# Kernel optimization log

Measured on AMD Instinct MI355X. Metric: run time of the kernel, lower is better.

Reference implementation:

```python
import jax, jax.numpy as jnp
import numpy as np

L, B, T, D, H = 8, 4, 1024, 1024, 16
DH = D // H
TPB, NB = 16, 64  # tokens_per_block, max_blocks; T == TPB*NB
EPS = 1e-5


def _block_causal_mask():
    idx = jnp.arange(T)
    causal = idx[:, None] >= idx[None, :]
    blk = idx // TPB
    block_diag = blk[:, None] == blk[None, :]
    return causal | block_diag  # [T, T] bool


def _ln(x, g, b):
    mu = jnp.mean(x, axis=-1, keepdims=True)
    var = jnp.mean(jnp.square(x - mu), axis=-1, keepdims=True)
    return (x - mu) * jax.lax.rsqrt(var + EPS) * g + b


def setup_inputs() -> dict:
    key = jax.random.key(0)
    ks = jax.random.split(key, 8)
    s = 0.02
    inp = {
        'sequences': jax.random.normal(ks[0], (B, T, D), jnp.float32),
        'Wq': jax.random.normal(ks[1], (L, D, D), jnp.float32) * s,
        'bq': jnp.zeros((L, D), jnp.float32),
        'Wk': jax.random.normal(ks[2], (L, D, D), jnp.float32) * s,
        'bk': jnp.zeros((L, D), jnp.float32),
        'Wv': jax.random.normal(ks[3], (L, D, D), jnp.float32) * s,
        'bv': jnp.zeros((L, D), jnp.float32),
        'Wp': jax.random.normal(ks[4], (L, D, D), jnp.float32) * s,
        'bp': jnp.zeros((L, D), jnp.float32),
        'ln1_g': jnp.ones((L, D), jnp.float32),
        'ln1_b': jnp.zeros((L, D), jnp.float32),
        'ln2_g': jnp.ones((L, D), jnp.float32),
        'ln2_b': jnp.zeros((L, D), jnp.float32),
        'W1': jax.random.normal(ks[5], (L, D, 4 * D), jnp.float32) * s,
        'b1': jnp.zeros((L, 4 * D), jnp.float32),
        'W2': jax.random.normal(ks[6], (L, 4 * D, D), jnp.float32) * s,
        'b2': jnp.zeros((L, D), jnp.float32),
        'lnf_g': jnp.ones((D,), jnp.float32),
        'lnf_b': jnp.zeros((D,), jnp.float32),
    }
    return inp


def reference(sequences, Wq, bq, Wk, bk, Wv, bv, Wp, bp,
              ln1_g, ln1_b, ln2_g, ln2_b, W1, b1, W2, b2, lnf_g, lnf_b):
    mask = _block_causal_mask()
    scale = 1.0 / np.sqrt(DH)
    x = sequences
    for i in range(L):
        h = _ln(x, ln1_g[i], ln1_b[i])
        q = (h @ Wq[i] + bq[i]).reshape(B, T, H, DH)
        k = (h @ Wk[i] + bk[i]).reshape(B, T, H, DH)
        v = (h @ Wv[i] + bv[i]).reshape(B, T, H, DH)
        att = jnp.einsum('bthd,bshd->bhts', q, k) * scale  # [B,H,T,T]
        att = jnp.where(mask, att, -jnp.inf)
        att = jax.nn.softmax(att, axis=-1)
        y = jnp.einsum('bhts,bshd->bthd', att, v).reshape(B, T, D)
        x = x + (y @ Wp[i] + bp[i])
        h2 = _ln(x, ln2_g[i], ln2_b[i])
        ff = jax.nn.gelu(h2 @ W1[i] + b1[i], approximate=False) @ W2[i] + b2[i]
        x = x + ff
    return _ln(x, lnf_g, lnf_b)
```

## Files before the change

kernel.cpp:

```cpp
#include <hip/hip_runtime.h>
#include <hip/hip_bf16.h>
#include <math.h>

#define B_ 4
#define T_ 1024
#define D_ 1024
#define H_ 16
#define DH_ 64
#define M_ 4096
#define QSTR_ 3072
#define EPS_ 1e-5f

typedef __attribute__((ext_vector_type(4))) float f32x4;
typedef __attribute__((ext_vector_type(8))) short s16x8;

#if __has_builtin(__builtin_amdgcn_exp2f)
#define EXP2F __builtin_amdgcn_exp2f
#else
#define EXP2F exp2f
#endif

__device__ __forceinline__ float gelu_f(float x) {
  return 0.5f * x * (1.0f + erff(x * 0.70710678118654752f));
}
__device__ __forceinline__ float b2f(unsigned short u) {
  union { unsigned int i; float f; } c; c.i = ((unsigned int)u) << 16; return c.f;
}
__device__ __forceinline__ unsigned short f2b(float f) {
  __hip_bfloat16 h = __float2bfloat16(f);
  return *reinterpret_cast<unsigned short*>(&h);
}
__device__ __forceinline__ void g2l16(void* l, const void* g) {
  __builtin_amdgcn_global_load_lds(
      (const __attribute__((address_space(1))) void*)g,
      (__attribute__((address_space(3))) void*)l, 16, 0, 0);
}

template<bool BF16OUT>
__global__ __launch_bounds__(256) void ln_kernel(
    const float* __restrict__ in, void* __restrict__ out,
    const float* __restrict__ g, const float* __restrict__ b) {
  const int row = blockIdx.x;
  const int tid = threadIdx.x;
  const float* rp = in + (size_t)row * D_;
  float4 v = *reinterpret_cast<const float4*>(rp + tid * 4);
  float s = v.x + v.y + v.z + v.w;
  float s2 = v.x * v.x + v.y * v.y + v.z * v.z + v.w * v.w;
#pragma unroll
  for (int off = 1; off < 64; off <<= 1) {
    s += __shfl_xor(s, off);
    s2 += __shfl_xor(s2, off);
  }
  __shared__ float red[2][4];
  const int wid = tid >> 6;
  if ((tid & 63) == 0) { red[0][wid] = s; red[1][wid] = s2; }
  __syncthreads();
  s = red[0][0] + red[0][1] + red[0][2] + red[0][3];
  s2 = red[1][0] + red[1][1] + red[1][2] + red[1][3];
  const float mu = s * (1.0f / D_);
  const float var = s2 * (1.0f / D_) - mu * mu;
  const float rs = rsqrtf(var + EPS_);
  float4 gv = *reinterpret_cast<const float4*>(g + tid * 4);
  float4 bv = *reinterpret_cast<const float4*>(b + tid * 4);
  float o0 = (v.x - mu) * rs * gv.x + bv.x;
  float o1 = (v.y - mu) * rs * gv.y + bv.y;
  float o2 = (v.z - mu) * rs * gv.z + bv.z;
  float o3 = (v.w - mu) * rs * gv.w + bv.w;
  if (BF16OUT) {
    ushort4 pk;
    pk.x = f2b(o0); pk.y = f2b(o1); pk.z = f2b(o2); pk.w = f2b(o3);
    *reinterpret_cast<ushort4*>((unsigned short*)out + (size_t)row * D_ + tid * 4) = pk;
  } else {
    *reinterpret_cast<float4*>((float*)out + (size_t)row * D_ + tid * 4) =
        make_float4(o0, o1, o2, o3);
  }
}

__global__ __launch_bounds__(256) void concat_bias(
    const float* __restrict__ bq, const float* __restrict__ bk,
    const float* __restrict__ bv, float* __restrict__ out) {
  const int i = blockIdx.x * 256 + threadIdx.x;
  const int l = i / QSTR_, c = i % QSTR_;
  const float* src = (c < 1024) ? bq : ((c < 2048) ? bk : bv);
  out[i] = src[l * 1024 + (c & 1023)];
}

__global__ __launch_bounds__(256) void reduce_add(
    float* __restrict__ x, const float* __restrict__ p) {
  const int i = blockIdx.x * 256 + threadIdx.x;
  float4 a = reinterpret_cast<float4*>(x)[i];
  float4 b = reinterpret_cast<const float4*>(p)[i];
  a.x += b.x; a.y += b.y; a.z += b.z; a.w += b.w;
  reinterpret_cast<float4*>(x)[i] = a;
}

__device__ __forceinline__ void transpose_tile(
    const float* __restrict__ src, int sld,
    __hip_bfloat16* __restrict__ dst, int dld, int k0, int n0) {
  __shared__ float tile[32][33];
  const int t = threadIdx.x;
  const int r = t >> 3;
  const int cq = (t & 7) * 4;
  float4 vv = *reinterpret_cast<const float4*>(src + (size_t)(k0 + r) * sld + n0 + cq);
  tile[r][cq + 0] = vv.x; tile[r][cq + 1] = vv.y;
  tile[r][cq + 2] = vv.z; tile[r][cq + 3] = vv.w;
  __syncthreads();
  ushort4 o;
  o.x = f2b(tile[cq + 0][r]); o.y = f2b(tile[cq + 1][r]);
  o.z = f2b(tile[cq + 2][r]); o.w = f2b(tile[cq + 3][r]);
  *reinterpret_cast<ushort4*>((unsigned short*)dst + (size_t)(n0 + r) * dld + k0 + cq) = o;
}

struct TrAll {
  const float *wq, *wk, *wv, *wp, *w1, *w2;
  __hip_bfloat16 *dqkv, *dp, *d1, *d2;
};

__global__ __launch_bounds__(256) void transpose_all(TrAll a) {
  const int t = blockIdx.x;
  const float* src;
  __hip_bfloat16* dst;
  int sld, dld, k0, n0;
  if (t < 4096) {
    const int m = t >> 10, tile = t & 1023;
    k0 = (tile >> 5) * 32; n0 = (tile & 31) * 32;
    src = (m == 0) ? a.wq : (m == 1) ? a.wk : (m == 2) ? a.wv : a.wp;
    sld = 1024; dld = 1024;
    dst = (m < 3) ? (a.dqkv + (size_t)m * 1024 * 1024) : a.dp;
  } else if (t < 8192) {
    const int tile = t - 4096;
    k0 = (tile & 31) * 32; n0 = (tile >> 5) * 32;
    src = a.w1; sld = 4096; dst = a.d1; dld = 1024;
  } else {
    const int tile = t - 8192;
    k0 = (tile >> 5) * 32; n0 = (tile & 31) * 32;
    src = a.w2; sld = 1024; dst = a.d2; dld = 4096;
  }
  transpose_tile(src, sld, dst, dld, k0, n0);
}

template<int MODE, int BN>
__global__ __launch_bounds__(256) void gemm_mfma(
    const __hip_bfloat16* __restrict__ A,
    const __hip_bfloat16* __restrict__ Bt,
    const float* __restrict__ bias,
    void* __restrict__ Cout, int N, int K) {
  __shared__ short As[3][128 * 32];
  __shared__ short Bs[3][BN * 32];
  int bid = blockIdx.y * gridDim.x + blockIdx.x;
  const int nwg = gridDim.x * gridDim.y;
  bid = (bid & 7) * (nwg >> 3) + (bid >> 3);
  const int gn = (bid % gridDim.x) * BN;
  const int gm = (bid / gridDim.x) * 128;

  const int tid = threadIdx.x;
  const int wid = tid >> 6, lane = tid & 63;
  constexpr int MR = (BN == 128) ? 4 : 2;
  const int wm = (BN == 128) ? (wid >> 1) : wid;
  const int wn = (BN == 128) ? (wid & 1) : 0;
  const int fr = lane & 15, kg = lane >> 4;

  const int ldr = lane >> 2;
  const int ldk = (((lane & 3) ^ ((lane >> 3) & 3)) * 8);
  const unsigned short* ap =
      (const unsigned short*)A + (size_t)(gm + wid * 32 + ldr) * K + ldk;
  const unsigned short* bp =
      (const unsigned short*)Bt +
      (size_t)(gn + ((BN == 128) ? wid * 32 : wid * 16) + ldr) * K + ldk;

  const int nkt = K >> 5;

#define STAGE_T(t, buf)                                                    \
  {                                                                        \
    const unsigned short* a_ = ap + (size_t)(t) * 32;                      \
    g2l16((char*)As[buf] + (wid * 2) * 1024, a_);                          \
    g2l16((char*)As[buf] + (wid * 2 + 1) * 1024, a_ + (size_t)16 * K);     \
    const unsigned short* b_ = bp + (size_t)(t) * 32;                      \
    if (BN == 128) {                                                       \
      g2l16((char*)Bs[buf] + (wid * 2) * 1024, b_);                        \
      g2l16((char*)Bs[buf] + (wid * 2 + 1) * 1024, b_ + (size_t)16 * K);   \
    } else {                                                               \
      g2l16((char*)Bs[buf] + wid * 1024, b_);                              \
    }                                                                      \
  }

  STAGE_T(0, 0);
  STAGE_T(1, 1);

  const int cxa = (kg ^ ((fr >> 1) & 3)) * 8;
  f32x4 acc[MR][4] = {};
  for (int t = 0; t < nkt; ++t) {
    const int buf = t % 3;
    if (t + 2 < nkt) STAGE_T(t + 2, (t + 2) % 3);
    const int rem = nkt - 1 - t;
    if (rem >= 2) {
      if (BN == 128) asm volatile("s_waitcnt vmcnt(8)" ::: "memory");
      else           asm volatile("s_waitcnt vmcnt(6)" ::: "memory");
    } else if (rem == 1) {
      if (BN == 128) asm volatile("s_waitcnt vmcnt(4)" ::: "memory");
      else           asm volatile("s_waitcnt vmcnt(3)" ::: "memory");
    } else {
      asm volatile("s_waitcnt vmcnt(0)" ::: "memory");
    }
    __builtin_amdgcn_s_barrier();
    __builtin_amdgcn_sched_barrier(0);
    s16x8 af[MR], bfr[4];
#pragma unroll
    for (int m = 0; m < MR; ++m)
      af[m] = *reinterpret_cast<const s16x8*>(
          &As[buf][(wm * (16 * MR) + m * 16 + fr) * 32 + cxa]);
#pragma unroll
    for (int n = 0; n < 4; ++n)
      bfr[n] = *reinterpret_cast<const s16x8*>(
          &Bs[buf][(wn * 64 + n * 16 + fr) * 32 + cxa]);
#pragma unroll
    for (int m = 0; m < MR; ++m)
#pragma unroll
      for (int n = 0; n < 4; ++n)
        acc[m][n] = __builtin_amdgcn_mfma_f32_16x16x32_bf16(af[m], bfr[n], acc[m][n], 0, 0, 0);
    __builtin_amdgcn_sched_barrier(0);
    __builtin_amdgcn_s_barrier();
  }
#undef STAGE_T

  const int r0 = gm + wm * (16 * MR);
  const int c0 = gn + wn * 64;
  float bb[4];
#pragma unroll
  for (int n = 0; n < 4; ++n)
    bb[n] = bias ? bias[c0 + n * 16 + fr] : 0.0f;
#pragma unroll
  for (int m = 0; m < MR; ++m) {
#pragma unroll
    for (int j = 0; j < 4; ++j) {
      const int row = r0 + m * 16 + kg * 4 + j;
#pragma unroll
      for (int n = 0; n < 4; ++n) {
        float val = acc[m][n][j] + bb[n];
        const size_t idx = (size_t)row * N + c0 + n * 16 + fr;
        if (MODE == 0) {
          ((unsigned short*)Cout)[idx] = f2b(val);
        } else if (MODE == 1) {
          float* cp = (float*)Cout + idx;
          *cp = *cp + val;
        } else {
          ((unsigned short*)Cout)[idx] = f2b(gelu_f(val));
        }
      }
    }
  }
}

__global__ __launch_bounds__(256) void gemm_sk2(
    const __hip_bfloat16* __restrict__ A,
    const __hip_bfloat16* __restrict__ Bt,
    const float* __restrict__ bias,
    float* __restrict__ X, float* __restrict__ P,
    int N, int K , int KS ) {
  __shared__ short As[3][128 * 32];
  __shared__ short Bs[3][64 * 32];
  int bid = blockIdx.y * gridDim.x + blockIdx.x;
  const int nwg = gridDim.x * gridDim.y;
  bid = (bid & 7) * (nwg >> 3) + (bid >> 3);
  const int gn = (bid % gridDim.x) * 64;
  const int gm = (bid / gridDim.x) * 128;
  const int koff = blockIdx.z * KS;

  const int tid = threadIdx.x;
  const int wid = tid >> 6, lane = tid & 63;
  const int wm = wid, wn = 0;
  const int fr = lane & 15, kg = lane >> 4;

  const int ldr = lane >> 2;
  const int ldk = (((lane & 3) ^ ((lane >> 3) & 3)) * 8);
  const unsigned short* ap =
      (const unsigned short*)A + (size_t)(gm + wid * 32 + ldr) * K + koff + ldk;
  const unsigned short* bp =
      (const unsigned short*)Bt + (size_t)(gn + wid * 16 + ldr) * K + koff + ldk;

  const int nkt = KS >> 5;

#define STAGE_S(t, buf)                                                    \
  {                                                                        \
    const unsigned short* a_ = ap + (size_t)(t) * 32;                      \
    g2l16((char*)As[buf] + (wid * 2) * 1024, a_);                          \
    g2l16((char*)As[buf] + (wid * 2 + 1) * 1024, a_ + (size_t)16 * K);     \
    g2l16((char*)Bs[buf] + wid * 1024, bp + (size_t)(t) * 32);             \
  }

  STAGE_S(0, 0);
  STAGE_S(1, 1);

  const int cxa = (kg ^ ((fr >> 1) & 3)) * 8;
  f32x4 acc[2][4] = {};
  for (int t = 0; t < nkt; ++t) {
    const int buf = t % 3;
    if (t + 2 < nkt) STAGE_S(t + 2, (t + 2) % 3);
    const int rem = nkt - 1 - t;
    if (rem >= 2)      asm volatile("s_waitcnt vmcnt(6)" ::: "memory");
    else if (rem == 1) asm volatile("s_waitcnt vmcnt(3)" ::: "memory");
    else               asm volatile("s_waitcnt vmcnt(0)" ::: "memory");
    __builtin_amdgcn_s_barrier();
    __builtin_amdgcn_sched_barrier(0);
    s16x8 af[2], bfr[4];
#pragma unroll
    for (int m = 0; m < 2; ++m)
      af[m] = *reinterpret_cast<const s16x8*>(
          &As[buf][(wm * 32 + m * 16 + fr) * 32 + cxa]);
#pragma unroll
    for (int n = 0; n < 4; ++n)
      bfr[n] = *reinterpret_cast<const s16x8*>(
          &Bs[buf][(wn * 64 + n * 16 + fr) * 32 + cxa]);
#pragma unroll
    for (int m = 0; m < 2; ++m)
#pragma unroll
      for (int n = 0; n < 4; ++n)
        acc[m][n] = __builtin_amdgcn_mfma_f32_16x16x32_bf16(af[m], bfr[n], acc[m][n], 0, 0, 0);
    __builtin_amdgcn_sched_barrier(0);
    __builtin_amdgcn_s_barrier();
  }
#undef STAGE_S

  const int r0 = gm + wm * 32;
  const int c0 = gn;
  if (blockIdx.z == 0) {
    float bb[4];
#pragma unroll
    for (int n = 0; n < 4; ++n) bb[n] = bias[c0 + n * 16 + fr];
#pragma unroll
    for (int m = 0; m < 2; ++m)
#pragma unroll
      for (int j = 0; j < 4; ++j) {
        const int row = r0 + m * 16 + kg * 4 + j;
#pragma unroll
        for (int n = 0; n < 4; ++n) {
          const size_t idx = (size_t)row * N + c0 + n * 16 + fr;
          X[idx] = X[idx] + acc[m][n][j] + bb[n];
        }
      }
  } else {
#pragma unroll
    for (int m = 0; m < 2; ++m)
#pragma unroll
      for (int j = 0; j < 4; ++j) {
        const int row = r0 + m * 16 + kg * 4 + j;
#pragma unroll
        for (int n = 0; n < 4; ++n) {
          const size_t idx = (size_t)row * N + c0 + n * 16 + fr;
          P[idx] = acc[m][n][j];
        }
      }
  }
}

__global__ __launch_bounds__(256) void attn_mfma(
    const __hip_bfloat16* __restrict__ qkv, __hip_bfloat16* __restrict__ yg) {
  const int qb = 7 - blockIdx.x;
  const int hh = blockIdx.y;
  const int bb = blockIdx.z;
  __shared__ short Qs[128 * 64];
  __shared__ short Ks[64 * 64];
  __shared__ short Vt[64 * 64];
  const int tid = threadIdx.x;
  const int wid = tid >> 6, lane = tid & 63;
  const int fr = lane & 15, kg = lane >> 4;
  const size_t qb_base = (size_t)bb * T_ * QSTR_ + (size_t)hh * DH_;
  const unsigned short* qgp = (const unsigned short*)qkv + qb_base;
  const unsigned short* kgp = qgp + 1024;
  const unsigned short* vgp = qgp + 2048;
  const float C = 0.125f * 1.4426950408889634f;

  {
    const int r8 = lane >> 3, cp = lane & 7;
#pragma unroll
    for (int u = 0; u < 4; ++u) {
      const int row = wid * 32 + u * 8 + r8;
      const int c16 = cp ^ (row & 7);
      g2l16((char*)Qs + (wid * 32 + u * 8) * 128,
            qgp + (size_t)(qb * 128 + row) * QSTR_ + c16 * 8);
    }
  }
  asm volatile("s_waitcnt vmcnt(0)" ::: "memory");
  __syncthreads();
  s16x8 qf[2][2];
#pragma unroll
  for (int rg = 0; rg < 2; ++rg) {
    const int row = wid * 32 + rg * 16 + fr;
    const char* rp = (const char*)Qs + row * 128;
    qf[rg][0] = *reinterpret_cast<const s16x8*>(rp + (((0 + kg) ^ (row & 7)) << 4));
    qf[rg][1] = *reinterpret_cast<const s16x8*>(rp + (((4 + kg) ^ (row & 7)) << 4));
  }

  f32x4 acco[2][4] = {};
  float m_run[2][4], l_run[2][4];
#pragma unroll
  for (int rg = 0; rg < 2; ++rg)
#pragma unroll
    for (int j = 0; j < 4; ++j) { m_run[rg][j] = -INFINITY; l_run[rg][j] = 0.f; }

  const int q16hi = qb * 8 + wid * 2 + 1;
  const int ntile = 2 * qb + 2;
  for (int kt = 0; kt < ntile; ++kt) {
    __syncthreads();
    {
      const int r8 = lane >> 3, cp = lane & 7;
#pragma unroll
      for (int u = 0; u < 2; ++u) {
        const int row = wid * 16 + u * 8 + r8;
        const int c16 = cp ^ (row & 7);
        g2l16((char*)Ks + (wid * 16 + u * 8) * 128,
              kgp + (size_t)(kt * 64 + row) * QSTR_ + c16 * 8);
      }
    }
    {
      const int kv0 = tid >> 3;
      const int d0 = (tid & 7) * 8;
      const int rot = tid & 7;
#pragma unroll
      for (int u = 0; u < 2; ++u) {
        const int kv = u * 32 + kv0;
        s16x8 sv = *reinterpret_cast<const s16x8*>(
            vgp + (size_t)(kt * 64 + kv) * QSTR_ + d0);
#pragma unroll
        for (int j = 0; j < 8; ++j) {
          const int jj = (j + rot) & 7;
          const int d = d0 + jj;
          *(short*)((char*)Vt + d * 128 + ((((kv >> 3) ^ jj) & 7) << 4) + (kv & 7) * 2) = sv[jj];
        }
      }
    }
    asm volatile("s_waitcnt vmcnt(0)" ::: "memory");
    __syncthreads();

    if (kt * 4 <= q16hi) {
      f32x4 accs[2][4] = {};
#pragma unroll
      for (int n = 0; n < 4; ++n) {
        const int row = n * 16 + fr;
        const char* rp = (const char*)Ks + row * 128;
        s16x8 kf0 = *reinterpret_cast<const s16x8*>(rp + (((0 + kg) ^ (row & 7)) << 4));
        s16x8 kf1 = *reinterpret_cast<const s16x8*>(rp + (((4 + kg) ^ (row & 7)) << 4));
#pragma unroll
        for (int rg = 0; rg < 2; ++rg) {
          accs[rg][n] = __builtin_amdgcn_mfma_f32_16x16x32_bf16(qf[rg][0], kf0, accs[rg][n], 0, 0, 0);
          accs[rg][n] = __builtin_amdgcn_mfma_f32_16x16x32_bf16(qf[rg][1], kf1, accs[rg][n], 0, 0, 0);
        }
      }
#pragma unroll
      for (int rg = 0; rg < 2; ++rg) {
        const int q16 = qb * 8 + wid * 2 + rg;
        float mloc[4] = {-3.0e38f, -3.0e38f, -3.0e38f, -3.0e38f};
#pragma unroll
        for (int n = 0; n < 4; ++n)
          if (kt * 4 + n <= q16)
#pragma unroll
            for (int j = 0; j < 4; ++j) mloc[j] = fmaxf(mloc[j], accs[rg][n][j]);
#pragma unroll
        for (int off = 1; off < 16; off <<= 1)
#pragma unroll
          for (int j = 0; j < 4; ++j) mloc[j] = fmaxf(mloc[j], __shfl_xor(mloc[j], off));
        float a_[4];
#pragma unroll
        for (int j = 0; j < 4; ++j) {
          const float mn = fmaxf(m_run[rg][j], mloc[j]);
          a_[j] = EXP2F((m_run[rg][j] - mn) * C);
          m_run[rg][j] = mn;
        }
        float psum[4] = {};
#pragma unroll
        for (int n = 0; n < 4; ++n) {
          const bool dead = (kt * 4 + n > q16);
          const int c16b = n * 2 + (fr >> 3);
#pragma unroll
          for (int j = 0; j < 4; ++j) {
            float p = dead ? 0.0f : EXP2F((accs[rg][n][j] - m_run[rg][j]) * C);
            psum[j] += p;
            const int row = wid * 32 + rg * 16 + kg * 4 + j;
            *(short*)((char*)Qs + row * 128 + (((c16b ^ (row & 7)) & 7) << 4) + (fr & 7) * 2) =
                (short)f2b(p);
          }
        }
#pragma unroll
        for (int j = 0; j < 4; ++j) l_run[rg][j] = l_run[rg][j] * a_[j] + psum[j];
#pragma unroll
        for (int dt = 0; dt < 4; ++dt)
#pragma unroll
          for (int j = 0; j < 4; ++j) acco[rg][dt][j] *= a_[j];
      }
#pragma unroll
      for (int rg = 0; rg < 2; ++rg) {
        const int prow = wid * 32 + rg * 16 + fr;
        const char* pp = (const char*)Qs + prow * 128;
#pragma unroll
        for (int kk = 0; kk < 2; ++kk) {
          const s16x8 pf = *reinterpret_cast<const s16x8*>(
              pp + ((((kk * 4 + kg) ^ (prow & 7)) & 7) << 4));
#pragma unroll
          for (int dt = 0; dt < 4; ++dt) {
            const int vrow = dt * 16 + fr;
            const s16x8 vf = *reinterpret_cast<const s16x8*>(
                (const char*)Vt + vrow * 128 + ((((kk * 4 + kg) ^ (vrow & 7)) & 7) << 4));
            acco[rg][dt] = __builtin_amdgcn_mfma_f32_16x16x32_bf16(pf, vf, acco[rg][dt], 0, 0, 0);
          }
        }
      }
    }
  }

#pragma unroll
  for (int off = 1; off < 16; off <<= 1)
#pragma unroll
    for (int rg = 0; rg < 2; ++rg)
#pragma unroll
      for (int j = 0; j < 4; ++j) l_run[rg][j] += __shfl_xor(l_run[rg][j], off);
  unsigned short* yp = (unsigned short*)yg + (size_t)bb * T_ * D_ + (size_t)hh * DH_;
#pragma unroll
  for (int rg = 0; rg < 2; ++rg) {
    float inv[4];
#pragma unroll
    for (int j = 0; j < 4; ++j) inv[j] = 1.0f / l_run[rg][j];
#pragma unroll
    for (int dt = 0; dt < 4; ++dt)
#pragma unroll
      for (int j = 0; j < 4; ++j) {
        const int row = qb * 128 + wid * 32 + rg * 16 + kg * 4 + j;
        yp[(size_t)row * D_ + dt * 16 + fr] = f2b(acco[rg][dt][j] * inv[j]);
      }
  }
}

extern "C" void kernel_launch(void* const* d_in, const int* in_sizes, int n_in,
                              void* d_out, int out_size, void* d_ws, size_t ws_size,
                              hipStream_t stream) {
  (void)in_sizes; (void)n_in; (void)out_size; (void)ws_size;
  const float* seq  = (const float*)d_in[0];
  const float* Wq   = (const float*)d_in[1];
  const float* bq   = (const float*)d_in[2];
  const float* Wk   = (const float*)d_in[3];
  const float* bk   = (const float*)d_in[4];
  const float* Wv   = (const float*)d_in[5];
  const float* bv   = (const float*)d_in[6];
  const float* Wp   = (const float*)d_in[7];
  const float* bp   = (const float*)d_in[8];
  const float* ln1g = (const float*)d_in[9];
  const float* ln1b = (const float*)d_in[10];
  const float* ln2g = (const float*)d_in[11];
  const float* ln2b = (const float*)d_in[12];
  const float* W1   = (const float*)d_in[13];
  const float* b1   = (const float*)d_in[14];
  const float* W2   = (const float*)d_in[15];
  const float* b2   = (const float*)d_in[16];
  const float* lnfg = (const float*)d_in[17];
  const float* lnfb = (const float*)d_in[18];

  float* x = (float*)d_out;
  char* ws = (char*)d_ws;
  const size_t MB = 1024ull * 1024ull;
  typedef __hip_bfloat16 bf16;
  bf16*  wtqkv = (bf16*)(ws + 0 * MB);
  bf16*  wtp   = (bf16*)(ws + 6 * MB);
  bf16*  wtF1  = (bf16*)(ws + 8 * MB);
  bf16*  wtF2  = (bf16*)(ws + 16 * MB);
  bf16*  hb    = (bf16*)(ws + 24 * MB);
  bf16*  qkv   = (bf16*)(ws + 32 * MB);
  bf16*  mid   = (bf16*)(ws + 56 * MB);
  float* bqkv  = (float*)(ws + 88 * MB);
  float* part  = (float*)(ws + 32 * MB);

  hipMemcpyAsync(x, seq, (size_t)M_ * D_ * sizeof(float), hipMemcpyDeviceToDevice, stream);

  const dim3 blk(256);
  concat_bias<<<96, blk, 0, stream>>>(bq, bk, bv, bqkv);

  for (int i = 0; i < 8; ++i) {
    const size_t wo  = (size_t)i * D_ * D_;
    const size_t vo  = (size_t)i * D_;
    const size_t w1o = (size_t)i * D_ * 4 * D_;

    ln_kernel<true><<<M_, blk, 0, stream>>>(x, hb, ln1g + vo, ln1b + vo);
    TrAll ta;
    ta.wq = Wq + wo; ta.wk = Wk + wo; ta.wv = Wv + wo; ta.wp = Wp + wo;
    ta.w1 = W1 + w1o; ta.w2 = W2 + w1o;
    ta.dqkv = wtqkv; ta.dp = wtp; ta.d1 = wtF1; ta.d2 = wtF2;
    transpose_all<<<12288, blk, 0, stream>>>(ta);
    gemm_mfma<0, 128><<<dim3(24, 32), blk, 0, stream>>>(
        hb, wtqkv, bqkv + (size_t)i * QSTR_, qkv, QSTR_, 1024);
    attn_mfma<<<dim3(8, 16, 4), blk, 0, stream>>>(qkv, hb);
    gemm_mfma<1, 64><<<dim3(16, 32), blk, 0, stream>>>(hb, wtp, bp + vo, x, 1024, 1024);
    ln_kernel<true><<<M_, blk, 0, stream>>>(x, hb, ln2g + vo, ln2b + vo);
    gemm_mfma<2, 128><<<dim3(32, 32), blk, 0, stream>>>(
        hb, wtF1, b1 + (size_t)i * 4096, mid, 4096, 1024);
    gemm_sk2<<<dim3(16, 32, 2), blk, 0, stream>>>(
        mid, wtF2, b2 + vo, x, part, 1024, 4096, 2048);
    reduce_add<<<4096, blk, 0, stream>>>(x, part);
  }
  ln_kernel<false><<<M_, blk, 0, stream>>>(x, x, lnfg, lnfb);
}
```

Before: 2.241 ms.

## Use wider 128x256 tile 512-thread GEMM for QKV and FFN projections

Replaces the QKV and FFN1 GEMMs, and the split-K FFN2 GEMM, with one templated kernel. It uses a 128x256 output tile per workgroup and 8 waves, each computing a 64x64 sub-tile. The larger tile raises arithmetic intensity and data reuse from LDS and cuts global traffic per FLOP. In exchange it uses more LDS and registers per block and launches fewer blocks, which may lower occupancy and hurt load balance across CUs.

```diff
diff --git a/kernel.cpp b/kernel.cpp
--- a/kernel.cpp
+++ b/kernel.cpp
@@ -251,105 +251,114 @@
   }
 }
 
-__global__ __launch_bounds__(256) void gemm_sk2(
+template<int MODE>
+__global__ __launch_bounds__(512) void gemm_w256(
     const __hip_bfloat16* __restrict__ A,
     const __hip_bfloat16* __restrict__ Bt,
     const float* __restrict__ bias,
-    float* __restrict__ X, float* __restrict__ P,
-    int N, int K , int KS ) {
+    void* __restrict__ Cout, float* __restrict__ P,
+    int N, int K, int KS) {
   __shared__ short As[3][128 * 32];
-  __shared__ short Bs[3][64 * 32];
+  __shared__ short Bs[3][256 * 32];
   int bid = blockIdx.y * gridDim.x + blockIdx.x;
   const int nwg = gridDim.x * gridDim.y;
   bid = (bid & 7) * (nwg >> 3) + (bid >> 3);
-  const int gn = (bid % gridDim.x) * 64;
+  const int gn = (bid % gridDim.x) * 256;
   const int gm = (bid / gridDim.x) * 128;
-  const int koff = blockIdx.z * KS;
+  const int koff = (MODE == 3) ? blockIdx.z * KS : 0;
 
   const int tid = threadIdx.x;
   const int wid = tid >> 6, lane = tid & 63;
-  const int wm = wid, wn = 0;
+  const int wm = wid & 1, wn = wid >> 1;
   const int fr = lane & 15, kg = lane >> 4;
 
   const int ldr = lane >> 2;
   const int ldk = (((lane & 3) ^ ((lane >> 3) & 3)) * 8);
   const unsigned short* ap =
-      (const unsigned short*)A + (size_t)(gm + wid * 32 + ldr) * K + koff + ldk;
+      (const unsigned short*)A + (size_t)(gm + wid * 16 + ldr) * K + koff + ldk;
   const unsigned short* bp =
-      (const unsigned short*)Bt + (size_t)(gn + wid * 16 + ldr) * K + koff + ldk;
-
-  const int nkt = KS >> 5;
-
-#define STAGE_S(t, buf)                                                    \
+      (const unsigned short*)Bt + (size_t)(gn + wid * 32 + ldr) * K + koff + ldk;
+
+  const int nkt = ((MODE == 3) ? KS : K) >> 5;
+
+#define STAGE_W(t, buf)                                                    \
   {                                                                        \
-    const unsigned short* a_ = ap + (size_t)(t) * 32;                      \
-    g2l16((char*)As[buf] + (wid * 2) * 1024, a_);                          \
-    g2l16((char*)As[buf] + (wid * 2 + 1) * 1024, a_ + (size_t)16 * K);     \
-    g2l16((char*)Bs[buf] + wid * 1024, bp + (size_t)(t) * 32);             \
-  }
-
-  STAGE_S(0, 0);
-  STAGE_S(1, 1);
+    g2l16((char*)As[buf] + wid * 1024, ap + (size_t)(t) * 32);             \
+    const unsigned short* b_ = bp + (size_t)(t) * 32;                      \
+    g2l16((char*)Bs[buf] + (wid * 2) * 1024, b_);                          \
+    g2l16((char*)Bs[buf] + (wid * 2 + 1) * 1024, b_ + (size_t)16 * K);     \
+  }
+
+  STAGE_W(0, 0);
+  STAGE_W(1, 1);
 
   const int cxa = (kg ^ ((fr >> 1) & 3)) * 8;
-  f32x4 acc[2][4] = {};
+  f32x4 acc[4][4] = {};
   for (int t = 0; t < nkt; ++t) {
     const int buf = t % 3;
-    if (t + 2 < nkt) STAGE_S(t + 2, (t + 2) % 3);
+    if (t + 2 < nkt) STAGE_W(t + 2, (t + 2) % 3);
     const int rem = nkt - 1 - t;
     if (rem >= 2)      asm volatile("s_waitcnt vmcnt(6)" ::: "memory");
     else if (rem == 1) asm volatile("s_waitcnt vmcnt(3)" ::: "memory");
     else               asm volatile("s_waitcnt vmcnt(0)" ::: "memory");
     __builtin_amdgcn_s_barrier();
     __builtin_amdgcn_sched_barrier(0);
-    s16x8 af[2], bfr[4];
-#pragma unroll
-    for (int m = 0; m < 2; ++m)
+    s16x8 af[4], bfr[4];
+#pragma unroll
+    for (int m = 0; m < 4; ++m)
       af[m] = *reinterpret_cast<const s16x8*>(
-          &As[buf][(wm * 32 + m * 16 + fr) * 32 + cxa]);
+          &As[buf][(wm * 64 + m * 16 + fr) * 32 + cxa]);
 #pragma unroll
     for (int n = 0; n < 4; ++n)
       bfr[n] = *reinterpret_cast<const s16x8*>(
           &Bs[buf][(wn * 64 + n * 16 + fr) * 32 + cxa]);
 #pragma unroll
-    for (int m = 0; m < 2; ++m)
+    for (int m = 0; m < 4; ++m)
 #pragma unroll
       for (int n = 0; n < 4; ++n)
         acc[m][n] = __builtin_amdgcn_mfma_f32_16x16x32_bf16(af[m], bfr[n], acc[m][n], 0, 0, 0);
     __builtin_amdgcn_sched_barrier(0);
     __builtin_amdgcn_s_barrier();
   }
-#undef STAGE_S
-
-  const int r0 = gm + wm * 32;
-  const int c0 = gn;
-  if (blockIdx.z == 0) {
-    float bb[4];
-#pragma unroll
-    for (int n = 0; n < 4; ++n) bb[n] = bias[c0 + n * 16 + fr];
-#pragma unroll
-    for (int m = 0; m < 2; ++m)
+#undef STAGE_W
+
+  const int r0 = gm + wm * 64;
+  const int c0 = gn + wn * 64;
+  if (MODE == 3 && blockIdx.z == 1) {
+#pragma unroll
+    for (int m = 0; m < 4; ++m)
 #pragma unroll
       for (int j = 0; j < 4; ++j) {
         const int row = r0 + m * 16 + kg * 4 + j;
 #pragma unroll
-        for (int n = 0; n < 4; ++n) {
-          const size_t idx = (size_t)row * N + c0 + n * 16 + fr;
-          X[idx] = X[idx] + acc[m][n][j] + bb[n];
+        for (int n = 0; n < 4; ++n)
+          P[(size_t)row * N + c0 + n * 16 + fr] = acc[m][n][j];
+      }
+    return;
+  }
+  float bb[4];
+#pragma unroll
+  for (int n = 0; n < 4; ++n)
+    bb[n] = bias ? bias[c0 + n * 16 + fr] : 0.0f;
+#pragma unroll
+  for (int m = 0; m < 4; ++m) {
+#pragma unroll
+    for (int j = 0; j < 4; ++j) {
+      const int row = r0 + m * 16 + kg * 4 + j;
+#pragma unroll
+      for (int n = 0; n < 4; ++n) {
+        float val = acc[m][n][j] + bb[n];
+        const size_t idx = (size_t)row * N + c0 + n * 16 + fr;
+        if (MODE == 0) {
+          ((unsigned short*)Cout)[idx] = f2b(val);
+        } else if (MODE == 1 || MODE == 3) {
+          float* cp = (float*)Cout + idx;
+          *cp = *cp + val;
+        } else {
+          ((unsigned short*)Cout)[idx] = f2b(gelu_f(val));
         }
       }
-  } else {
-#pragma unroll
-    for (int m = 0; m < 2; ++m)
-#pragma unroll
-      for (int j = 0; j < 4; ++j) {
-        const int row = r0 + m * 16 + kg * 4 + j;
-#pragma unroll
-        for (int n = 0; n < 4; ++n) {
-          const size_t idx = (size_t)row * N + c0 + n * 16 + fr;
-          P[idx] = acc[m][n][j];
-        }
-      }
+    }
   }
 }
 
@@ -570,6 +579,7 @@
   hipMemcpyAsync(x, seq, (size_t)M_ * D_ * sizeof(float), hipMemcpyDeviceToDevice, stream);
 
   const dim3 blk(256);
+  const dim3 blkw(512);
   concat_bias<<<96, blk, 0, stream>>>(bq, bk, bv, bqkv);
 
   for (int i = 0; i < 8; ++i) {
@@ -583,14 +593,14 @@
     ta.w1 = W1 + w1o; ta.w2 = W2 + w1o;
     ta.dqkv = wtqkv; ta.dp = wtp; ta.d1 = wtF1; ta.d2 = wtF2;
     transpose_all<<<12288, blk, 0, stream>>>(ta);
-    gemm_mfma<0, 128><<<dim3(24, 32), blk, 0, stream>>>(
-        hb, wtqkv, bqkv + (size_t)i * QSTR_, qkv, QSTR_, 1024);
+    gemm_w256<0><<<dim3(12, 32), blkw, 0, stream>>>(
+        hb, wtqkv, bqkv + (size_t)i * QSTR_, qkv, nullptr, QSTR_, 1024, 0);
     attn_mfma<<<dim3(8, 16, 4), blk, 0, stream>>>(qkv, hb);
     gemm_mfma<1, 64><<<dim3(16, 32), blk, 0, stream>>>(hb, wtp, bp + vo, x, 1024, 1024);
     ln_kernel<true><<<M_, blk, 0, stream>>>(x, hb, ln2g + vo, ln2b + vo);
-    gemm_mfma<2, 128><<<dim3(32, 32), blk, 0, stream>>>(
-        hb, wtF1, b1 + (size_t)i * 4096, mid, 4096, 1024);
-    gemm_sk2<<<dim3(16, 32, 2), blk, 0, stream>>>(
+    gemm_w256<2><<<dim3(16, 32), blkw, 0, stream>>>(
+        hb, wtF1, b1 + (size_t)i * 4096, mid, nullptr, 4096, 1024, 0);
+    gemm_w256<3><<<dim3(4, 32, 2), blkw, 0, stream>>>(
         mid, wtF2, b2 + vo, x, part, 1024, 4096, 2048);
     reduce_add<<<4096, blk, 0, stream>>>(x, part);
   }
```

New measurement: 2.171 ms. 1.03x faster.
